# Kernel optimization log

Measured on AMD Instinct MI355X. Metric: run time of the kernel, lower is better.

## Reference

```python
import jax, jax.numpy as jnp
import numpy as np

EMB = 128
HID = 4 * 32  # 4*hidden_dim = 128
N_NODES = 100000
N_EDGES = 800000


def setup_inputs() -> dict:
    key = jax.random.key(0)
    k1, k2, k3, k4 = jax.random.split(key, 4)
    node_emb = jax.random.normal(k1, (N_NODES, EMB), dtype=jnp.float32)
    edge_index = jax.random.randint(k2, (2, N_EDGES), 0, N_NODES, dtype=jnp.int64)
    # xavier_uniform for Linear weights, zeros bias; LayerNorm gamma=1, beta=0
    lim1 = float(np.sqrt(6.0 / (2 * EMB + HID)))
    W1 = jax.random.uniform(k3, (2 * EMB, HID), minval=-lim1, maxval=lim1, dtype=jnp.float32)
    b1 = jnp.zeros((HID,), dtype=jnp.float32)
    ln_g = jnp.ones((HID,), dtype=jnp.float32)
    ln_b = jnp.zeros((HID,), dtype=jnp.float32)
    lim2 = float(np.sqrt(6.0 / (HID + 1)))
    W2 = jax.random.uniform(k4, (HID, 1), minval=-lim2, maxval=lim2, dtype=jnp.float32)
    b2 = jnp.zeros((1,), dtype=jnp.float32)
    return {"node_emb": node_emb, "edge_index": edge_index,
            "W1": W1, "b1": b1, "ln_g": ln_g, "ln_b": ln_b, "W2": W2, "b2": b2}


def reference(node_emb, edge_index, W1, b1, ln_g, ln_b, W2, b2):
    src, dst = edge_index[0], edge_index[1]
    # gather + concat: [E, 2*EMB]
    edge_emb = jnp.concatenate([node_emb[src], node_emb[dst]], axis=1)
    h = edge_emb @ W1 + b1  # [E, HID]
    # LayerNorm over last dim (eps=1e-5, torch default)
    mu = jnp.mean(h, axis=-1, keepdims=True)
    var = jnp.var(h, axis=-1, keepdims=True)
    h = (h - mu) * jax.lax.rsqrt(var + 1e-5) * ln_g + ln_b
    h = jax.nn.relu(h)  # Dropout is identity in eval mode
    w = jax.nn.sigmoid(h @ W2 + b2)  # [E, 1]
    w = jnp.nan_to_num(w, nan=0.5)
    return w
```

## Files before the change

### kernel.cpp

```cpp
#include <hip/hip_runtime.h>
#include <hip/hip_bf16.h>
#include <math.h>

#define EMB 128
#define HID 128
#define NCOL 256

typedef __attribute__((ext_vector_type(8))) short short8v;
typedef __attribute__((ext_vector_type(4))) float f32x4;

__device__ __forceinline__ unsigned short f2bf(float f) {
    union { float f; unsigned int u; } v; v.f = f;
    unsigned int r = (v.u + 0x7FFFu + ((v.u >> 16) & 1u)) >> 16;
    return (unsigned short)r;
}

__global__ __launch_bounds__(256) void w_prep(
    const float* __restrict__ W1, unsigned short* __restrict__ Wt)
{
    int idx = blockIdx.x * 256 + threadIdx.x;
    int c = idx >> 7;
    int k = idx & 127;
    float v = W1[(size_t)(k + ((c >> 7) << 7)) * HID + (c & 127)];
    Wt[idx] = f2bf(v);
}

__global__ __launch_bounds__(256) void proj_mfma(
    const float* __restrict__ A,
    const unsigned short* __restrict__ Wt,
    unsigned short* __restrict__ P,
    int N, int nTiles)
{
    const int w    = threadIdx.x >> 6;
    const int lane = threadIdx.x & 63;
    const int l16  = lane & 15;
    const int lk   = lane >> 4;

    short8v afrag[4][4];
#pragma unroll
    for (int cf = 0; cf < 4; ++cf)
#pragma unroll
        for (int ks = 0; ks < 4; ++ks) {
            int c = 64 * w + 16 * cf + l16;
            afrag[cf][ks] = *(const short8v*)(Wt + (size_t)c * EMB + 32 * ks + 8 * lk);
        }

    for (int t = blockIdx.x; t < nTiles; t += gridDim.x) {
        const int n0   = t * 16;
        int node = n0 + l16;
        int nc   = node < N ? node : N - 1;
        const float* ap = A + (size_t)nc * EMB + 8 * lk;

        short8v bf[4];
#pragma unroll
        for (int ks = 0; ks < 4; ++ks) {
            float4 a0 = *(const float4*)(ap + 32 * ks);
            float4 a1 = *(const float4*)(ap + 32 * ks + 4);
            short8v f = { (short)f2bf(a0.x), (short)f2bf(a0.y), (short)f2bf(a0.z), (short)f2bf(a0.w),
                          (short)f2bf(a1.x), (short)f2bf(a1.y), (short)f2bf(a1.z), (short)f2bf(a1.w) };
            bf[ks] = f;
        }

        f32x4 acc[4];
#pragma unroll
        for (int cf = 0; cf < 4; ++cf) acc[cf] = (f32x4)0.0f;

#pragma unroll
        for (int ks = 0; ks < 4; ++ks)
#pragma unroll
            for (int cf = 0; cf < 4; ++cf)
                acc[cf] = __builtin_amdgcn_mfma_f32_16x16x32_bf16(
                    afrag[cf][ks], bf[ks], acc[cf], 0, 0, 0);

        if (node < N) {
            unsigned short* prow = P + (size_t)node * NCOL;
#pragma unroll
            for (int cf = 0; cf < 4; ++cf) {
                unsigned int u0 = (unsigned int)f2bf(acc[cf][0]) |
                                  ((unsigned int)f2bf(acc[cf][1]) << 16);
                unsigned int u1 = (unsigned int)f2bf(acc[cf][2]) |
                                  ((unsigned int)f2bf(acc[cf][3]) << 16);
                uint2 v = make_uint2(u0, u1);
                *(uint2*)(prow + 64 * w + 16 * cf + 4 * lk) = v;
            }
        }
    }
}

__global__ __launch_bounds__(256) void edge_kernel(
    const unsigned short* __restrict__ P,
    const int* __restrict__ ei,
    const float* __restrict__ b1,
    const float* __restrict__ lng,
    const float* __restrict__ lnb,
    const float* __restrict__ W2,
    const float* __restrict__ b2,
    float* __restrict__ out, int E)
{
    const int l16 = threadIdx.x & 15;
    const int c0  = l16 * 8;

    float vb1[8], vg[8], vbt[8], vw2[8];
#pragma unroll
    for (int i = 0; i < 8; i += 4) {
        *(float4*)&vb1[i] = *(const float4*)(b1  + c0 + i);
        *(float4*)&vg[i]  = *(const float4*)(lng + c0 + i);
        *(float4*)&vbt[i] = *(const float4*)(lnb + c0 + i);
        *(float4*)&vw2[i] = *(const float4*)(W2  + c0 + i);
    }
    const float bias2 = b2[0];

    int slot   = blockIdx.x * (blockDim.x >> 4) + (threadIdx.x >> 4);
    int nslots = gridDim.x * (blockDim.x >> 4);

    for (int e = slot; e < E; e += nslots) {
        int src = ei[e];
        int dst = ei[E + e];
        uint4 us = *(const uint4*)(P + (size_t)src * NCOL + c0);
        uint4 ud = *(const uint4*)(P + (size_t)dst * NCOL + HID + c0);

        float h[8];
        {
            unsigned int uu[4] = {us.x, us.y, us.z, us.w};
            unsigned int dd[4] = {ud.x, ud.y, ud.z, ud.w};
#pragma unroll
            for (int j = 0; j < 4; ++j) {
                float a0 = __uint_as_float(uu[j] << 16);
                float a1 = __uint_as_float(uu[j] & 0xFFFF0000u);
                float d0 = __uint_as_float(dd[j] << 16);
                float d1 = __uint_as_float(dd[j] & 0xFFFF0000u);
                h[2 * j]     = a0 + d0 + vb1[2 * j];
                h[2 * j + 1] = a1 + d1 + vb1[2 * j + 1];
            }
        }
        float s = 0.0f, sq = 0.0f;
#pragma unroll
        for (int i = 0; i < 8; ++i) {
            s += h[i];
            sq = fmaf(h[i], h[i], sq);
        }
#pragma unroll
        for (int m = 8; m >= 1; m >>= 1) {
            s  += __shfl_xor(s,  m, 16);
            sq += __shfl_xor(sq, m, 16);
        }
        float mu  = s * (1.0f / HID);
        float var = sq * (1.0f / HID) - mu * mu;
        float r   = rsqrtf(var + 1e-5f);
        float nmr = -mu * r;

        float z = 0.0f;
#pragma unroll
        for (int i = 0; i < 8; ++i) {
            float t = fmaf(h[i], r, nmr);
            float y = fmaf(t, vg[i], vbt[i]);
            y = fmaxf(y, 0.0f);
            z = fmaf(y, vw2[i], z);
        }
#pragma unroll
        for (int m = 8; m >= 1; m >>= 1) z += __shfl_xor(z, m, 16);

        if (l16 == 0) {
            float zz = z + bias2;
            float wv = 1.0f / (1.0f + expf(-zz));
            if (wv != wv) wv = 0.5f;
            out[e] = wv;
        }
    }
}

__global__ __launch_bounds__(256) void fused_kernel(
    const float* __restrict__ X,
    const int* __restrict__ ei,
    const float* __restrict__ W1,
    const float* __restrict__ b1,
    const float* __restrict__ lng,
    const float* __restrict__ lnb,
    const float* __restrict__ W2,
    const float* __restrict__ b2,
    float* __restrict__ out, int E)
{
    const int lane = threadIdx.x & 31;
    const int c0   = lane * 4;
    const float4 vb1 = *(const float4*)(b1  + c0);
    const float4 vg  = *(const float4*)(lng + c0);
    const float4 vbt = *(const float4*)(lnb + c0);
    const float4 vw2 = *(const float4*)(W2  + c0);
    const float bias2 = b2[0];

    int slot   = blockIdx.x * (blockDim.x >> 5) + (threadIdx.x >> 5);
    int nslots = gridDim.x * (blockDim.x >> 5);

    for (int e = slot; e < E; e += nslots) {
        int src = ei[e];
        int dst = ei[E + e];
        const float* xs = X + (size_t)src * EMB;
        const float* xd = X + (size_t)dst * EMB;
        float h0 = vb1.x, h1 = vb1.y, h2 = vb1.z, h3 = vb1.w;
        for (int k = 0; k < EMB; ++k) {
            float a  = xs[k];
            float4 w = *(const float4*)(W1 + (size_t)k * HID + c0);
            h0 = fmaf(a, w.x, h0); h1 = fmaf(a, w.y, h1);
            h2 = fmaf(a, w.z, h2); h3 = fmaf(a, w.w, h3);
        }
        for (int k = 0; k < EMB; ++k) {
            float a  = xd[k];
            float4 w = *(const float4*)(W1 + (size_t)(EMB + k) * HID + c0);
            h0 = fmaf(a, w.x, h0); h1 = fmaf(a, w.y, h1);
            h2 = fmaf(a, w.z, h2); h3 = fmaf(a, w.w, h3);
        }
        float s  = h0 + h1 + h2 + h3;
        float sq = h0 * h0 + h1 * h1 + h2 * h2 + h3 * h3;
#pragma unroll
        for (int m = 16; m >= 1; m >>= 1) {
            s  += __shfl_xor(s,  m, 32);
            sq += __shfl_xor(sq, m, 32);
        }
        float mu  = s * (1.0f / HID);
        float var = sq * (1.0f / HID) - mu * mu;
        float r   = rsqrtf(var + 1e-5f);
        float y0 = fmaxf(fmaf((h0 - mu) * r, vg.x, vbt.x), 0.0f);
        float y1 = fmaxf(fmaf((h1 - mu) * r, vg.y, vbt.y), 0.0f);
        float y2 = fmaxf(fmaf((h2 - mu) * r, vg.z, vbt.z), 0.0f);
        float y3 = fmaxf(fmaf((h3 - mu) * r, vg.w, vbt.w), 0.0f);
        float z = y0 * vw2.x + y1 * vw2.y + y2 * vw2.z + y3 * vw2.w;
#pragma unroll
        for (int m = 16; m >= 1; m >>= 1) z += __shfl_xor(z, m, 32);
        if (lane == 0) {
            float zz = z + bias2;
            float wv = 1.0f / (1.0f + expf(-zz));
            if (wv != wv) wv = 0.5f;
            out[e] = wv;
        }
    }
}

extern "C" void kernel_launch(void* const* d_in, const int* in_sizes, int n_in,
                              void* d_out, int out_size, void* d_ws, size_t ws_size,
                              hipStream_t stream) {
    const float* node_emb = (const float*)d_in[0];
    const int*   ei       = (const int*)d_in[1];
    const float* W1       = (const float*)d_in[2];
    const float* b1       = (const float*)d_in[3];
    const float* lng      = (const float*)d_in[4];
    const float* lnb      = (const float*)d_in[5];
    const float* W2       = (const float*)d_in[6];
    const float* b2       = (const float*)d_in[7];
    float* out = (float*)d_out;

    const int N = in_sizes[0] / EMB;
    const int E = in_sizes[1] / 2;

    const size_t pBytes = (size_t)N * NCOL * sizeof(unsigned short);
    const size_t need   = pBytes + (size_t)NCOL * EMB * sizeof(unsigned short);

    if (ws_size >= need) {
        unsigned short* P  = (unsigned short*)d_ws;
        unsigned short* Wt = (unsigned short*)((char*)d_ws + pBytes);

        w_prep<<<(NCOL * EMB) / 256, 256, 0, stream>>>(W1, Wt);

        int nTiles = (N + 15) / 16;
        int gridP  = nTiles < 2048 ? nTiles : 2048;
        proj_mfma<<<gridP, 256, 0, stream>>>(node_emb, Wt, P, N, nTiles);

        edge_kernel<<<2048, 256, 0, stream>>>(P, ei, b1, lng, lnb, W2, b2, out, E);
    } else {
        fused_kernel<<<2048, 256, 0, stream>>>(node_emb, ei, W1, b1, lng, lnb,
                                               W2, b2, out, E);
    }
}
```

Baseline: 198.0 us.

## Use DPP row reductions, fold bias into projection, prefetch node tiles

The edge kernel's 16-lane LayerNorm and output reductions now use DPP quad-permute and row-mirror adds instead of `__shfl_xor` shuffles. The b1 bias is added in the projection kernel before bf16 packing, so the edge kernel no longer loads or adds it. The projection kernel software-prefetches the next tile's node embeddings into registers while the current tile's MFMAs run. The edge kernel grid is doubled to 4096 blocks. The aim is to cut cross-lane shuffle latency and per-edge ALU work, and to hide load latency in the projection. The cost is more registers, and rounding the summed projection plus bias to bf16 is a small numeric difference.

```diff
diff --git a/kernel.cpp b/kernel.cpp
--- a/kernel.cpp
+++ b/kernel.cpp
@@ -13,6 +13,22 @@
     union { float f; unsigned int u; } v; v.f = f;
     unsigned int r = (v.u + 0x7FFFu + ((v.u >> 16) & 1u)) >> 16;
     return (unsigned short)r;
+}
+__device__ __forceinline__ float bf2f(unsigned int u16) {
+    return __uint_as_float(u16 << 16);
+}
+
+template<int CTRL>
+__device__ __forceinline__ float dpp_add(float x) {
+    int y = __builtin_amdgcn_update_dpp(0, __float_as_int(x), CTRL, 0xf, 0xf, true);
+    return x + __int_as_float(y);
+}
+__device__ __forceinline__ float red16(float x) {
+    x = dpp_add<0xB1>(x);
+    x = dpp_add<0x4E>(x);
+    x = dpp_add<0x141>(x);
+    x = dpp_add<0x140>(x);
+    return x;
 }
 
 __global__ __launch_bounds__(256) void w_prep(
@@ -28,6 +44,7 @@
 __global__ __launch_bounds__(256) void proj_mfma(
     const float* __restrict__ A,
     const unsigned short* __restrict__ Wt,
+    const float* __restrict__ b1,
     unsigned short* __restrict__ P,
     int N, int nTiles)
 {
@@ -45,22 +62,50 @@
             afrag[cf][ks] = *(const short8v*)(Wt + (size_t)c * EMB + 32 * ks + 8 * lk);
         }
 
-    for (int t = blockIdx.x; t < nTiles; t += gridDim.x) {
-        const int n0   = t * 16;
-        int node = n0 + l16;
+    float4 b1v[4];
+#pragma unroll
+    for (int cf = 0; cf < 4; ++cf) {
+        if (w < 2) b1v[cf] = *(const float4*)(b1 + 64 * w + 16 * cf + 4 * lk);
+        else       b1v[cf] = make_float4(0.f, 0.f, 0.f, 0.f);
+    }
+
+    int t = blockIdx.x;
+    if (t >= nTiles) return;
+
+    float4 fbuf[8];
+    {
+        int node = t * 16 + l16;
         int nc   = node < N ? node : N - 1;
         const float* ap = A + (size_t)nc * EMB + 8 * lk;
-
+#pragma unroll
+        for (int ks = 0; ks < 4; ++ks) {
+            fbuf[2 * ks]     = *(const float4*)(ap + 32 * ks);
+            fbuf[2 * ks + 1] = *(const float4*)(ap + 32 * ks + 4);
+        }
+    }
+
+    for (; t < nTiles; t += gridDim.x) {
         short8v bf[4];
 #pragma unroll
         for (int ks = 0; ks < 4; ++ks) {
-            float4 a0 = *(const float4*)(ap + 32 * ks);
-            float4 a1 = *(const float4*)(ap + 32 * ks + 4);
+            float4 a0 = fbuf[2 * ks], a1 = fbuf[2 * ks + 1];
             short8v f = { (short)f2bf(a0.x), (short)f2bf(a0.y), (short)f2bf(a0.z), (short)f2bf(a0.w),
                           (short)f2bf(a1.x), (short)f2bf(a1.y), (short)f2bf(a1.z), (short)f2bf(a1.w) };
             bf[ks] = f;
         }
 
+        int tn = t + gridDim.x;
+        if (tn < nTiles) {
+            int node = tn * 16 + l16;
+            int nc   = node < N ? node : N - 1;
+            const float* ap = A + (size_t)nc * EMB + 8 * lk;
+#pragma unroll
+            for (int ks = 0; ks < 4; ++ks) {
+                fbuf[2 * ks]     = *(const float4*)(ap + 32 * ks);
+                fbuf[2 * ks + 1] = *(const float4*)(ap + 32 * ks + 4);
+            }
+        }
+
         f32x4 acc[4];
 #pragma unroll
         for (int cf = 0; cf < 4; ++cf) acc[cf] = (f32x4)0.0f;
@@ -72,16 +117,18 @@
                 acc[cf] = __builtin_amdgcn_mfma_f32_16x16x32_bf16(
                     afrag[cf][ks], bf[ks], acc[cf], 0, 0, 0);
 
+        int node = t * 16 + l16;
         if (node < N) {
             unsigned short* prow = P + (size_t)node * NCOL;
 #pragma unroll
             for (int cf = 0; cf < 4; ++cf) {
-                unsigned int u0 = (unsigned int)f2bf(acc[cf][0]) |
-                                  ((unsigned int)f2bf(acc[cf][1]) << 16);
-                unsigned int u1 = (unsigned int)f2bf(acc[cf][2]) |
-                                  ((unsigned int)f2bf(acc[cf][3]) << 16);
-                uint2 v = make_uint2(u0, u1);
-                *(uint2*)(prow + 64 * w + 16 * cf + 4 * lk) = v;
+                float v0 = acc[cf][0] + b1v[cf].x;
+                float v1 = acc[cf][1] + b1v[cf].y;
+                float v2 = acc[cf][2] + b1v[cf].z;
+                float v3 = acc[cf][3] + b1v[cf].w;
+                unsigned int u0 = (unsigned int)f2bf(v0) | ((unsigned int)f2bf(v1) << 16);
+                unsigned int u1 = (unsigned int)f2bf(v2) | ((unsigned int)f2bf(v3) << 16);
+                *(uint2*)(prow + 64 * w + 16 * cf + 4 * lk) = make_uint2(u0, u1);
             }
         }
     }
@@ -90,7 +137,6 @@
 __global__ __launch_bounds__(256) void edge_kernel(
     const unsigned short* __restrict__ P,
     const int* __restrict__ ei,
-    const float* __restrict__ b1,
     const float* __restrict__ lng,
     const float* __restrict__ lnb,
     const float* __restrict__ W2,
@@ -100,10 +146,9 @@
     const int l16 = threadIdx.x & 15;
     const int c0  = l16 * 8;
 
-    float vb1[8], vg[8], vbt[8], vw2[8];
+    float vg[8], vbt[8], vw2[8];
 #pragma unroll
     for (int i = 0; i < 8; i += 4) {
-        *(float4*)&vb1[i] = *(const float4*)(b1  + c0 + i);
         *(float4*)&vg[i]  = *(const float4*)(lng + c0 + i);
         *(float4*)&vbt[i] = *(const float4*)(lnb + c0 + i);
         *(float4*)&vw2[i] = *(const float4*)(W2  + c0 + i);
@@ -125,12 +170,9 @@
             unsigned int dd[4] = {ud.x, ud.y, ud.z, ud.w};
 #pragma unroll
             for (int j = 0; j < 4; ++j) {
-                float a0 = __uint_as_float(uu[j] << 16);
-                float a1 = __uint_as_float(uu[j] & 0xFFFF0000u);
-                float d0 = __uint_as_float(dd[j] << 16);
-                float d1 = __uint_as_float(dd[j] & 0xFFFF0000u);
-                h[2 * j]     = a0 + d0 + vb1[2 * j];
-                h[2 * j + 1] = a1 + d1 + vb1[2 * j + 1];
+                h[2 * j]     = bf2f(uu[j] & 0xFFFFu) + bf2f(dd[j] & 0xFFFFu);
+                h[2 * j + 1] = __uint_as_float(uu[j] & 0xFFFF0000u) +
+                               __uint_as_float(dd[j] & 0xFFFF0000u);
             }
         }
         float s = 0.0f, sq = 0.0f;
@@ -139,11 +181,9 @@
             s += h[i];
             sq = fmaf(h[i], h[i], sq);
         }
-#pragma unroll
-        for (int m = 8; m >= 1; m >>= 1) {
-            s  += __shfl_xor(s,  m, 16);
-            sq += __shfl_xor(sq, m, 16);
-        }
+        s  = red16(s);
+        sq = red16(sq);
+
         float mu  = s * (1.0f / HID);
         float var = sq * (1.0f / HID) - mu * mu;
         float r   = rsqrtf(var + 1e-5f);
@@ -157,8 +197,7 @@
             y = fmaxf(y, 0.0f);
             z = fmaf(y, vw2[i], z);
         }
-#pragma unroll
-        for (int m = 8; m >= 1; m >>= 1) z += __shfl_xor(z, m, 16);
+        z = red16(z);
 
         if (l16 == 0) {
             float zz = z + bias2;
@@ -262,9 +301,9 @@
 
         int nTiles = (N + 15) / 16;
         int gridP  = nTiles < 2048 ? nTiles : 2048;
-        proj_mfma<<<gridP, 256, 0, stream>>>(node_emb, Wt, P, N, nTiles);
-
-        edge_kernel<<<2048, 256, 0, stream>>>(P, ei, b1, lng, lnb, W2, b2, out, E);
+        proj_mfma<<<gridP, 256, 0, stream>>>(node_emb, Wt, b1, P, N, nTiles);
+
+        edge_kernel<<<4096, 256, 0, stream>>>(P, ei, lng, lnb, W2, b2, out, E);
     } else {
         fused_kernel<<<2048, 256, 0, stream>>>(node_emb, ei, W1, b1, lng, lnb,
                                                W2, b2, out, E);
```

New measurement: 198.0 us. No clear change (+0.0%).
